# Performance work log

Hardware: AMD Instinct MI355X
Metric: run time of the kernel (lower is better)

## Reference

```python
import jax, jax.numpy as jnp
import numpy as np

# hyperparameters (from init_kwargs / repo defaults)
AMP_COEF = 1.0
ARG_COEF = 1.0
SSIM_COEF = 1.0
BETA = 1.0
STFT_COEF = 1e-4
EPS = 1e-8
STFT_F = 12
STFT_S = 4


def _gauss_kernel(size=11, sigma=1.5):
    x = jnp.arange(size, dtype=jnp.float32) - (size - 1) / 2.0
    g = jnp.exp(-0.5 * (x / sigma) ** 2)
    k = jnp.outer(g, g)
    return k / jnp.sum(k)


def _depthwise_filter(img, k):
    # img: [B,H,W,C]; 11x11 gaussian, VALID padding, depthwise (per-channel)
    c = img.shape[-1]
    kern = jnp.tile(k[:, :, None, None], (1, 1, 1, c))  # HWIO, I=1, O=C
    return jax.lax.conv_general_dilated(
        img, kern, (1, 1), 'VALID',
        dimension_numbers=('NHWC', 'HWIO', 'NHWC'),
        feature_group_count=c)


def ssim(x, y, max_val=1.0):
    # faithful to tf.image.ssim defaults: filter 11, sigma 1.5, k1=0.01, k2=0.03
    c1 = (0.01 * max_val) ** 2
    c2 = (0.03 * max_val) ** 2
    k = _gauss_kernel()
    mu_x = _depthwise_filter(x, k)
    mu_y = _depthwise_filter(y, k)
    var_x = _depthwise_filter(x * x, k) - mu_x * mu_x
    var_y = _depthwise_filter(y * y, k) - mu_y * mu_y
    cov = _depthwise_filter(x * y, k) - mu_x * mu_y
    lum = (2.0 * mu_x * mu_y + c1) / (mu_x * mu_x + mu_y * mu_y + c1)
    cs = (2.0 * cov + c2) / (var_x + var_y + c2)
    return jnp.mean(lum * cs, axis=(1, 2, 3))  # [B]


def stft(image, f=STFT_F, s=STFT_S):
    # image: [B,N,N,C] -> batched patchwise 2D FFT, cropped to [:f//2,:f//2]
    n = image.shape[1]
    p = (n - f) // s + 1          # num_conv per axis
    half = f // 2
    rows = (jnp.arange(p) * s)[:, None] + jnp.arange(f)   # [P, f]
    patches = image[:, rows]                              # [B,P,f,N,C]
    patches = patches[:, :, :, rows]                      # [B,P,f,P,f,C]
    patches = jnp.transpose(patches, (0, 1, 3, 2, 4, 5))  # [B,Pi,Pj,f,f,C]
    b, c = image.shape[0], image.shape[-1]
    patches = patches.reshape(b, p * p, f, f, c)          # k = i*P + j ordering
    fft = jnp.fft.fft2(patches.astype(jnp.complex64), axes=(2, 3))
    return fft[:, :, :half, :half, :]                     # [B,P*P,half,half,C]


def _freq_filter(f=STFT_F):
    lin = jnp.linspace(0.0, 1.0, f // 2)[:, None]
    return (lin * lin.T)[:, :, None]                      # [half,half,1]


def setup_inputs() -> dict:
    key = jax.random.key(0)
    k1, k2, k3, k4 = jax.random.split(key, 4)
    B, N, C, L = 32, 160, 3, 128
    return {
        'mean': jax.random.normal(k1, (B, L), dtype=jnp.float32),
        'logvar': jax.random.normal(k2, (B, L), dtype=jnp.float32),
        'x_in': jax.random.uniform(k3, (B, N, N, C), dtype=jnp.float32),
        'x_out': jax.random.uniform(k4, (B, N, N, C), dtype=jnp.float32),
    }


def reference(mean, logvar, x_in, x_out):
    # KLD per sample
    var = jnp.exp(logvar)
    kld = -0.5 * jnp.sum(1.0 + logvar - var - mean * mean, axis=1)  # [B]
    # SSIM recon term
    recons = SSIM_COEF * ssim(x_in, x_out, 1.0)                     # [B]
    # patchwise STFT amp/phase loss ('ours')
    stft_out = stft(x_out, STFT_F, STFT_S)
    stft_in = stft(x_in, STFT_F, STFT_S)
    ff = _freq_filter(STFT_F)                                       # [half,half,1]
    arg_diff = jnp.abs(jnp.angle(stft_out + EPS) - jnp.angle(stft_in + EPS))
    amp_diff = jnp.abs(jnp.abs(stft_out) - jnp.abs(stft_in))
    arg_loss = jnp.sum(arg_diff * ff, axis=(1, 2, 3, 4))            # [B]
    amp_loss = jnp.sum(amp_diff * ff, axis=(1, 2, 3, 4))            # [B]
    stft_loss = ARG_COEF * arg_loss + AMP_COEF * amp_loss
    loss = jnp.mean(BETA * kld + recons + STFT_COEF * stft_loss)
    return loss
```

## Files before the change

kernel.cpp:

```cpp
#include <hip/hip_runtime.h>
#include <hip/hip_fp16.h>
#include <math.h>

#define BATCH 32
#define NPIX 160
#define LDIM 128
#define OUT_SZ 150

#define THREADS 512
#define N_BLOCKS 1825
#define RD_OFF   2880
#define VPMU_OFF 2880
#define VPVV_OFF 4192
#define VPXY_OFF 5504
#define VROWSTR  164
#define SMEM_FLOATS 8960

__device__ constexpr float TWC[12] = { 1.f, 0.86602540f, 0.5f, 0.f, -0.5f, -0.86602540f,
                                      -1.f,-0.86602540f,-0.5f, 0.f,  0.5f,  0.86602540f};
__device__ constexpr float TWS[12] = { 0.f,-0.5f,-0.86602540f,-1.f,-0.86602540f,-0.5f,
                                       0.f, 0.5f, 0.86602540f, 1.f, 0.86602540f, 0.5f};

__device__ constexpr float GW[11] = {0.00102838f, 0.00759876f, 0.03600076f, 0.10936070f,
                                     0.21300554f, 0.26601172f, 0.21300554f, 0.10936070f,
                                     0.03600076f, 0.00759876f, 0.00102838f};

__device__ __forceinline__ float fast_atan2f(float y, float x) {
    float ax = fabsf(x), ay = fabsf(y);
    float mx = fmaxf(ax, ay), mn = fminf(ax, ay);
    float z = mn * __builtin_amdgcn_rcpf(mx);
    float z2 = z * z;
    float p = fmaf(z2, -0.01172120f, 0.05265332f);
    p = fmaf(z2, p, -0.11643287f);
    p = fmaf(z2, p, 0.19354346f);
    p = fmaf(z2, p, -0.33262347f);
    p = fmaf(z2, p, 0.99997726f);
    p = p * z;
    if (ay > ax) p = 1.57079632679489662f - p;
    if (x < 0.f) p = 3.14159265358979323f - p;
    return (y < 0.f) ? -p : p;
}

__device__ __forceinline__ __half2 h2swap(__half2 v) {
    unsigned u;
    __builtin_memcpy(&u, &v, 4);
    u = (u >> 16) | (u << 16);
    __half2 r;
    __builtin_memcpy(&r, &u, 4);
    return r;
}

__device__ __forceinline__ float4 extract_c(float4 f0, float4 f1, float4 f2, int c) {
    if (c == 0) return make_float4(f0.x, f0.w, f1.z, f2.y);
    if (c == 1) return make_float4(f0.y, f1.x, f1.w, f2.z);
    return make_float4(f0.z, f1.y, f2.x, f2.w);
}

__global__ __launch_bounds__(THREADS) void work_kernel(const float* __restrict__ xin,
                                                       const float* __restrict__ xout,
                                                       const float* __restrict__ mean,
                                                       const float* __restrict__ logvar,
                                                       float* __restrict__ out) {
    __shared__ __align__(16) float SMEM[SMEM_FLOATS];
    __shared__ float sm8[8];
    const int tid = threadIdx.x;
    const int gid = blockIdx.x;
    float acc = 0.f;

    if (gid == 1824) {
        float a = 0.f;
        for (int i = tid; i < BATCH * LDIM; i += THREADS) {
            float m = mean[i], lv = logvar[i];
            a += -0.5f * (1.f + lv - expf(lv) - m * m) * (1.f / 32.f);
        }
        #pragma unroll
        for (int o = 32; o > 0; o >>= 1) a += __shfl_down(a, o, 64);
        if ((tid & 63) == 0) sm8[tid >> 6] = a;
        __syncthreads();
        if (tid == 0) {
            float s = sm8[0];
            #pragma unroll
            for (int i = 1; i < 8; ++i) s += sm8[i];
            atomicAdd(out, s);
        }
        return;
    }

    int idx  = (gid & 7) * 228 + (gid >> 3);
    int b    = idx / 57;
    int rem  = idx % 57;
    int tile = (rem / 3);
    int c    = rem % 3;
    int r0 = tile * 8;
    __half2* HXY = (__half2*)SMEM;
    __half2* RD  = (__half2*)(SMEM + RD_OFF);
    const __half2 hz = __float2half2_rn(0.f);

    for (int t = tid; t < 720; t += THREADS) {
        int rr = t / 40;
        int cq = t % 40;
        int row = r0 + rr;
        float4 xa = make_float4(0.f, 0.f, 0.f, 0.f);
        float4 xb = make_float4(0.f, 0.f, 0.f, 0.f);
        if (row < NPIX) {
            size_t off = ((size_t)(b * 160 + row) * 160 + cq * 4) * 3;
            const float4* qa = (const float4*)(xin + off);
            const float4* qb = (const float4*)(xout + off);
            float4 a0 = qa[0], a1 = qa[1], a2 = qa[2];
            float4 b0 = qb[0], b1 = qb[1], b2 = qb[2];
            xa = extract_c(a0, a1, a2, c);
            xb = extract_c(b0, b1, b2, c);
        }
        __half2 h[4] __attribute__((aligned(16)));
        h[0] = __floats2half2_rn(xa.x, xb.x);
        h[1] = __floats2half2_rn(xa.y, xb.y);
        h[2] = __floats2half2_rn(xa.z, xb.z);
        h[3] = __floats2half2_rn(xa.w, xb.w);
        *(float4*)&HXY[rr * 160 + cq * 4] = *(float4*)h;
    }
    __syncthreads();

    for (int t = tid; t < 608; t += THREADS) {
        int pc = t % 38;
        int r  = t / 38;
        float4 raw[3];
        raw[0] = *(const float4*)&HXY[r * 160 + pc * 4];
        raw[1] = *(const float4*)&HXY[r * 160 + pc * 4 + 4];
        raw[2] = *(const float4*)&HXY[r * 160 + pc * 4 + 8];
        const __half2* x = (const __half2*)raw;
        __half2 ev[5], ov[5];
        #pragma unroll
        for (int j = 1; j <= 5; ++j) {
            ev[j-1] = __hadd2(x[j], x[12 - j]);
            ov[j-1] = __hsub2(x[j], x[12 - j]);
        }
        __half2* dst = &RD[(r * 38 + pc) * 10];
        #pragma unroll
        for (int vv = 0; vv < 5; ++vv) {
            const int v = vv + 1;
            __half2 re = (v & 1) ? __hsub2(x[0], x[6]) : __hadd2(x[0], x[6]);
            __half2 im = hz;
            #pragma unroll
            for (int j = 1; j <= 5; ++j) {
                const int kk = (v * j) % 12;
                re = __hfma2(ev[j-1], __float2half2_rn(TWC[kk]), re);
                im = __hfma2(ov[j-1], __float2half2_rn(TWS[kk]), im);
            }
            __half2 w2[2] __attribute__((aligned(8)));
            w2[0] = re;
            w2[1] = im;
            *(float2*)&dst[vv * 2] = *(float2*)w2;
        }
    }
    __syncthreads();

    if (tid < 380) {
        int pc = tid % 38;
        int vv = (tid / 38) % 5;
        int g  = tid / 190;
        __half2 FR[5], FI[5];
        #pragma unroll
        for (int uu = 0; uu < 5; ++uu) { FR[uu] = hz; FI[uu] = hz; }
        #pragma unroll
        for (int i = 0; i < 6; ++i) {
            int rlo = 4 * g + i, rhi = rlo + 6;
            __half2 lo[2] __attribute__((aligned(8)));
            __half2 hi[2] __attribute__((aligned(8)));
            *(float2*)lo = *(const float2*)&RD[(rlo * 38 + pc) * 10 + vv * 2];
            *(float2*)hi = *(const float2*)&RD[(rhi * 38 + pc) * 10 + vv * 2];
            __half2 spR = __hadd2(lo[0], hi[0]), smR = __hsub2(lo[0], hi[0]);
            __half2 spI = __hadd2(lo[1], hi[1]), smI = __hsub2(lo[1], hi[1]);
            #pragma unroll
            for (int uu = 0; uu < 5; ++uu) {
                const int u = uu + 1;
                const int kk = (u * i) % 12;
                __half2 sR = (u & 1) ? smR : spR;
                __half2 sI = (u & 1) ? smI : spI;
                FR[uu] = __hfma2(sR, __float2half2_rn(TWC[kk]),
                         __hfma2(sI, __float2half2_rn(-TWS[kk]), FR[uu]));
                FI[uu] = __hfma2(sI, __float2half2_rn(TWC[kk]),
                         __hfma2(sR, __float2half2_rn(TWS[kk]), FI[uu]));
            }
        }
        float sacc = 0.f;
        #pragma unroll
        for (int uu = 0; uu < 5; ++uu) {
            float2 fr = __half22float2(FR[uu]);
            float2 fi = __half22float2(FI[uu]);
            float aI = fast_atan2f(fi.x, fr.x + 1e-8f);
            float aO = fast_atan2f(fi.y, fr.y + 1e-8f);
            float mI = __builtin_amdgcn_sqrtf(fmaf(fr.x, fr.x, fi.x * fi.x));
            float mO = __builtin_amdgcn_sqrtf(fmaf(fr.y, fr.y, fi.y * fi.y));
            float ff = (float)((uu + 1) * (vv + 1)) * 0.04f;
            sacc += ff * (fabsf(aO - aI) + fabsf(mO - mI));
        }
        acc += sacc * (1e-4f / 32.f);
    }
    __syncthreads();

    for (int t = tid; t < 320; t += THREADS) {
        int orow = t / 40;
        int cbase = (t % 40) * 4;
        __half2 amu[4], avv[4], axy[4];
        #pragma unroll
        for (int o = 0; o < 4; ++o) { amu[o] = hz; avv[o] = hz; axy[o] = hz; }
        #pragma unroll
        for (int kk = 0; kk < 11; ++kk) {
            float4 raw = *(const float4*)&HXY[(orow + kk) * 160 + cbase];
            const __half2* h = (const __half2*)&raw;
            const __half2 w2 = __float2half2_rn(GW[kk]);
            #pragma unroll
            for (int o = 0; o < 4; ++o) {
                __half2 t2 = __hmul2(w2, h[o]);
                amu[o] = __hadd2(amu[o], t2);
                avv[o] = __hfma2(t2, h[o], avv[o]);
                axy[o] = __hfma2(t2, h2swap(h[o]), axy[o]);
            }
        }
        int base = orow * VROWSTR + cbase;
        *(float4*)&SMEM[VPMU_OFF + base] = *(float4*)amu;
        *(float4*)&SMEM[VPVV_OFF + base] = *(float4*)avv;
        *(float4*)&SMEM[VPXY_OFF + base] = make_float4(
            __low2float(axy[0]), __low2float(axy[1]),
            __low2float(axy[2]), __low2float(axy[3]));
    }
    __syncthreads();

    {
        float hacc = 0.f;
        for (int t = tid; t < 600; t += THREADS) {
            int orow = t / 75;
            int oc = (t % 75) * 2;
            int base = orow * VROWSTR + oc;
            __half2 m[12], s0 = hz, s1 = hz;
            #pragma unroll
            for (int q = 0; q < 6; ++q)
                *(float2*)&m[2 * q] = *(const float2*)&SMEM[VPMU_OFF + base + 2 * q];
            #pragma unroll
            for (int kk = 0; kk < 11; ++kk) {
                const __half2 w2 = __float2half2_rn(GW[kk]);
                s0 = __hfma2(w2, m[kk],     s0);
                s1 = __hfma2(w2, m[kk + 1], s1);
            }
            float2 mu0 = __half22float2(s0);
            float2 mu1 = __half22float2(s1);
            __half2 v0 = hz, v1 = hz;
            #pragma unroll
            for (int q = 0; q < 6; ++q)
                *(float2*)&m[2 * q] = *(const float2*)&SMEM[VPVV_OFF + base + 2 * q];
            #pragma unroll
            for (int kk = 0; kk < 11; ++kk) {
                const __half2 w2 = __float2half2_rn(GW[kk]);
                v0 = __hfma2(w2, m[kk],     v0);
                v1 = __hfma2(w2, m[kk + 1], v1);
            }
            float2 vv0 = __half22float2(v0);
            float2 vv1 = __half22float2(v1);
            float zs[12];
            #pragma unroll
            for (int q = 0; q < 6; ++q) {
                float2 y2 = *(const float2*)&SMEM[VPXY_OFF + base + 2 * q];
                zs[2 * q] = y2.x; zs[2 * q + 1] = y2.y;
            }
            float xy0 = 0.f, xy1 = 0.f;
            #pragma unroll
            for (int kk = 0; kk < 11; ++kk) {
                xy0 = fmaf(GW[kk], zs[kk],     xy0);
                xy1 = fmaf(GW[kk], zs[kk + 1], xy1);
            }
            if (r0 + orow < OUT_SZ) {
                const float c1 = 1e-4f, c2 = 9e-4f;
                #pragma unroll
                for (int o = 0; o < 2; ++o) {
                    float mx = o ? mu1.x : mu0.x, my = o ? mu1.y : mu0.y;
                    float ex = o ? vv1.x : vv0.x, ey = o ? vv1.y : vv0.y;
                    float cv = (o ? xy1 : xy0) - mx * my;
                    float vx = ex - mx * mx;
                    float vy = ey - my * my;
                    float lum = (2.f * mx * my + c1) *
                                __builtin_amdgcn_rcpf(fmaf(mx, mx, my * my) + c1);
                    float cs  = (2.f * cv + c2) *
                                __builtin_amdgcn_rcpf(vx + vy + c2);
                    hacc += lum * cs;
                }
            }
        }
        acc += hacc * (1.f / (32.f * 150.f * 150.f * 3.f));
    }

    #pragma unroll
    for (int o = 32; o > 0; o >>= 1) acc += __shfl_down(acc, o, 64);
    if ((tid & 63) == 0) sm8[tid >> 6] = acc;
    __syncthreads();
    if (tid == 0) {
        float s = sm8[0];
        #pragma unroll
        for (int i = 1; i < 8; ++i) s += sm8[i];
        atomicAdd(out, s);
    }
}

extern "C" void kernel_launch(void* const* d_in, const int* in_sizes, int n_in,
                              void* d_out, int out_size, void* d_ws, size_t ws_size,
                              hipStream_t stream) {
    const float* mean   = (const float*)d_in[0];
    const float* logvar = (const float*)d_in[1];
    const float* xin    = (const float*)d_in[2];
    const float* xout   = (const float*)d_in[3];
    float* out = (float*)d_out;

    hipMemsetAsync(out, 0, sizeof(float), stream);
    work_kernel<<<N_BLOCKS, THREADS, 0, stream>>>(xin, xout, mean, logvar, out);
}
```

Baseline: 105.2 us.

## Give each wavefront private shared-memory scratch and drop block-wide barriers between stages

After the block-wide load of the tile into shared memory, each wavefront now owns a fixed slice of patch columns and one SSIM output row. Each wavefront uses its own private shared-memory workspace, so the row-DFT, column-DFT, vertical and horizontal blur stages need only compiler memory fences instead of __syncthreads. The HXY row stride is padded to 164 to reduce bank conflicts. The phase difference is now taken from one atan2 of the conjugate product with wrap correction instead of two atan2 calls. This cuts barrier stalls and transcendental work, but the uneven per-wave work split (5 vs 4 columns) may leave some lanes idle, and relying on wave-synchronous execution without explicit wave barriers is a correctness risk.

```diff
diff --git a/kernel.cpp b/kernel.cpp
--- a/kernel.cpp
+++ b/kernel.cpp
@@ -9,12 +9,13 @@
 
 #define THREADS 512
 #define N_BLOCKS 1825
-#define RD_OFF   2880
-#define VPMU_OFF 2880
-#define VPVV_OFF 4192
-#define VPXY_OFF 5504
-#define VROWSTR  164
-#define SMEM_FLOATS 8960
+
+#define HXYSTR 164
+#define HXY_SZ (18 * HXYSTR)
+#define SMEM_FLOATS (HXY_SZ + 6 * 800 + 2 * 640)
+#define VP_MU 0
+#define VP_VV 160
+#define VP_XY 320
 
 __device__ constexpr float TWC[12] = { 1.f, 0.86602540f, 0.5f, 0.f, -0.5f, -0.86602540f,
                                       -1.f,-0.86602540f,-0.5f, 0.f,  0.5f,  0.86602540f};
@@ -89,11 +90,17 @@
     int idx  = (gid & 7) * 228 + (gid >> 3);
     int b    = idx / 57;
     int rem  = idx % 57;
-    int tile = (rem / 3);
+    int tile = rem / 3;
     int c    = rem % 3;
     int r0 = tile * 8;
+
     __half2* HXY = (__half2*)SMEM;
-    __half2* RD  = (__half2*)(SMEM + RD_OFF);
+    const int wid  = tid >> 6;
+    const int lane = tid & 63;
+    const int npcl = (wid < 6) ? 5 : 4;
+    const int pc0  = (wid < 6) ? wid * 5 : 30 + (wid - 6) * 4;
+    float*   WS  = SMEM + HXY_SZ + ((wid < 6) ? wid * 800 : 4800 + (wid - 6) * 640);
+    __half2* RDW = (__half2*)WS;
     const __half2 hz = __float2half2_rn(0.f);
 
     for (int t = tid; t < 720; t += THREADS) {
@@ -116,17 +123,19 @@
         h[1] = __floats2half2_rn(xa.y, xb.y);
         h[2] = __floats2half2_rn(xa.z, xb.z);
         h[3] = __floats2half2_rn(xa.w, xb.w);
-        *(float4*)&HXY[rr * 160 + cq * 4] = *(float4*)h;
+        *(float4*)&HXY[rr * HXYSTR + cq * 4] = *(float4*)h;
     }
     __syncthreads();
 
-    for (int t = tid; t < 608; t += THREADS) {
-        int pc = t % 38;
-        int r  = t / 38;
+    for (int t = lane; t < 16 * npcl; t += 64) {
+        int r, pcl;
+        if (npcl == 5) { r = t / 5;  pcl = t - r * 5; }
+        else           { r = t >> 2; pcl = t & 3; }
+        int pc = pc0 + pcl;
         float4 raw[3];
-        raw[0] = *(const float4*)&HXY[r * 160 + pc * 4];
-        raw[1] = *(const float4*)&HXY[r * 160 + pc * 4 + 4];
-        raw[2] = *(const float4*)&HXY[r * 160 + pc * 4 + 8];
+        raw[0] = *(const float4*)&HXY[r * HXYSTR + pc * 4];
+        raw[1] = *(const float4*)&HXY[r * HXYSTR + pc * 4 + 4];
+        raw[2] = *(const float4*)&HXY[r * HXYSTR + pc * 4 + 8];
         const __half2* x = (const __half2*)raw;
         __half2 ev[5], ov[5];
         #pragma unroll
@@ -134,7 +143,6 @@
             ev[j-1] = __hadd2(x[j], x[12 - j]);
             ov[j-1] = __hsub2(x[j], x[12 - j]);
         }
-        __half2* dst = &RD[(r * 38 + pc) * 10];
         #pragma unroll
         for (int vv = 0; vv < 5; ++vv) {
             const int v = vv + 1;
@@ -149,64 +157,75 @@
             __half2 w2[2] __attribute__((aligned(8)));
             w2[0] = re;
             w2[1] = im;
-            *(float2*)&dst[vv * 2] = *(float2*)w2;
-        }
-    }
-    __syncthreads();
-
-    if (tid < 380) {
-        int pc = tid % 38;
-        int vv = (tid / 38) % 5;
-        int g  = tid / 190;
-        __half2 FR[5], FI[5];
-        #pragma unroll
-        for (int uu = 0; uu < 5; ++uu) { FR[uu] = hz; FI[uu] = hz; }
-        #pragma unroll
-        for (int i = 0; i < 6; ++i) {
-            int rlo = 4 * g + i, rhi = rlo + 6;
-            __half2 lo[2] __attribute__((aligned(8)));
-            __half2 hi[2] __attribute__((aligned(8)));
-            *(float2*)lo = *(const float2*)&RD[(rlo * 38 + pc) * 10 + vv * 2];
-            *(float2*)hi = *(const float2*)&RD[(rhi * 38 + pc) * 10 + vv * 2];
-            __half2 spR = __hadd2(lo[0], hi[0]), smR = __hsub2(lo[0], hi[0]);
-            __half2 spI = __hadd2(lo[1], hi[1]), smI = __hsub2(lo[1], hi[1]);
+            *(float2*)&RDW[((r * 5 + vv) * npcl + pcl) * 2] = *(float2*)w2;
+        }
+    }
+    asm volatile("" ::: "memory");
+
+    {
+        int g = lane >> 5, j = lane & 31;
+        if (j < 5 * npcl) {
+            int vvq, pcl;
+            if (npcl == 5) { vvq = j / 5;  pcl = j - vvq * 5; }
+            else           { vvq = j >> 2; pcl = j & 3; }
+            __half2 FR[5], FI[5];
+            #pragma unroll
+            for (int uu = 0; uu < 5; ++uu) { FR[uu] = hz; FI[uu] = hz; }
+            #pragma unroll
+            for (int i = 0; i < 6; ++i) {
+                int rlo = 4 * g + i, rhi = rlo + 6;
+                __half2 lo[2] __attribute__((aligned(8)));
+                __half2 hi[2] __attribute__((aligned(8)));
+                *(float2*)lo = *(const float2*)&RDW[((rlo * 5 + vvq) * npcl + pcl) * 2];
+                *(float2*)hi = *(const float2*)&RDW[((rhi * 5 + vvq) * npcl + pcl) * 2];
+                __half2 spR = __hadd2(lo[0], hi[0]), smR = __hsub2(lo[0], hi[0]);
+                __half2 spI = __hadd2(lo[1], hi[1]), smI = __hsub2(lo[1], hi[1]);
+                #pragma unroll
+                for (int uu = 0; uu < 5; ++uu) {
+                    const int u = uu + 1;
+                    const int kk = (u * i) % 12;
+                    __half2 sR = (u & 1) ? smR : spR;
+                    __half2 sI = (u & 1) ? smI : spI;
+                    FR[uu] = __hfma2(sR, __float2half2_rn(TWC[kk]),
+                             __hfma2(sI, __float2half2_rn(-TWS[kk]), FR[uu]));
+                    FI[uu] = __hfma2(sI, __float2half2_rn(TWC[kk]),
+                             __hfma2(sR, __float2half2_rn(TWS[kk]), FI[uu]));
+                }
+            }
+            float sacc = 0.f;
             #pragma unroll
             for (int uu = 0; uu < 5; ++uu) {
-                const int u = uu + 1;
-                const int kk = (u * i) % 12;
-                __half2 sR = (u & 1) ? smR : spR;
-                __half2 sI = (u & 1) ? smI : spI;
-                FR[uu] = __hfma2(sR, __float2half2_rn(TWC[kk]),
-                         __hfma2(sI, __float2half2_rn(-TWS[kk]), FR[uu]));
-                FI[uu] = __hfma2(sI, __float2half2_rn(TWC[kk]),
-                         __hfma2(sR, __float2half2_rn(TWS[kk]), FI[uu]));
-            }
-        }
-        float sacc = 0.f;
-        #pragma unroll
-        for (int uu = 0; uu < 5; ++uu) {
-            float2 fr = __half22float2(FR[uu]);
-            float2 fi = __half22float2(FI[uu]);
-            float aI = fast_atan2f(fi.x, fr.x + 1e-8f);
-            float aO = fast_atan2f(fi.y, fr.y + 1e-8f);
-            float mI = __builtin_amdgcn_sqrtf(fmaf(fr.x, fr.x, fi.x * fi.x));
-            float mO = __builtin_amdgcn_sqrtf(fmaf(fr.y, fr.y, fi.y * fi.y));
-            float ff = (float)((uu + 1) * (vv + 1)) * 0.04f;
-            sacc += ff * (fabsf(aO - aI) + fabsf(mO - mI));
-        }
-        acc += sacc * (1e-4f / 32.f);
-    }
-    __syncthreads();
-
-    for (int t = tid; t < 320; t += THREADS) {
-        int orow = t / 40;
-        int cbase = (t % 40) * 4;
+                float2 fr = __half22float2(FR[uu]);
+                float2 fi = __half22float2(FI[uu]);
+                float rb = fr.x + 1e-8f, ib = fi.x;
+                float ra = fr.y + 1e-8f, ia = fi.y;
+                float re_p = fmaf(ra, rb, ia * ib);
+                float im_p = fmaf(ia, rb, -(ra * ib));
+                float w  = fast_atan2f(im_p, re_p);
+                float aw = fabsf(w);
+                float alt = 6.28318530717958648f - aw;
+                bool sa = (ia < 0.f), sb = (ib < 0.f);
+                float adiff = (sa == sb) ? aw
+                             : (((w >= 0.f) == !sa) ? aw : alt);
+                float mI = __builtin_amdgcn_sqrtf(fmaf(fr.x, fr.x, fi.x * fi.x));
+                float mO = __builtin_amdgcn_sqrtf(fmaf(fr.y, fr.y, fi.y * fi.y));
+                float ff = (float)((uu + 1) * (vvq + 1)) * 0.04f;
+                sacc += ff * (adiff + fabsf(mO - mI));
+            }
+            acc += sacc * (1e-4f / 32.f);
+        }
+    }
+    asm volatile("" ::: "memory");
+
+    if (lane < 40) {
+        const int orow = wid;
+        int cbase = lane * 4;
         __half2 amu[4], avv[4], axy[4];
         #pragma unroll
         for (int o = 0; o < 4; ++o) { amu[o] = hz; avv[o] = hz; axy[o] = hz; }
         #pragma unroll
         for (int kk = 0; kk < 11; ++kk) {
-            float4 raw = *(const float4*)&HXY[(orow + kk) * 160 + cbase];
+            float4 raw = *(const float4*)&HXY[(orow + kk) * HXYSTR + cbase];
             const __half2* h = (const __half2*)&raw;
             const __half2 w2 = __float2half2_rn(GW[kk]);
             #pragma unroll
@@ -217,25 +236,22 @@
                 axy[o] = __hfma2(t2, h2swap(h[o]), axy[o]);
             }
         }
-        int base = orow * VROWSTR + cbase;
-        *(float4*)&SMEM[VPMU_OFF + base] = *(float4*)amu;
-        *(float4*)&SMEM[VPVV_OFF + base] = *(float4*)avv;
-        *(float4*)&SMEM[VPXY_OFF + base] = make_float4(
+        *(float4*)&WS[VP_MU + cbase] = *(float4*)amu;
+        *(float4*)&WS[VP_VV + cbase] = *(float4*)avv;
+        *(float4*)&WS[VP_XY + cbase] = make_float4(
             __low2float(axy[0]), __low2float(axy[1]),
             __low2float(axy[2]), __low2float(axy[3]));
     }
-    __syncthreads();
-
-    {
+    asm volatile("" ::: "memory");
+
+    if (r0 + wid < OUT_SZ) {
         float hacc = 0.f;
-        for (int t = tid; t < 600; t += THREADS) {
-            int orow = t / 75;
-            int oc = (t % 75) * 2;
-            int base = orow * VROWSTR + oc;
+        for (int t = lane; t < 75; t += 64) {
+            int oc = t * 2;
             __half2 m[12], s0 = hz, s1 = hz;
             #pragma unroll
             for (int q = 0; q < 6; ++q)
-                *(float2*)&m[2 * q] = *(const float2*)&SMEM[VPMU_OFF + base + 2 * q];
+                *(float2*)&m[2 * q] = *(const float2*)&WS[VP_MU + oc + 2 * q];
             #pragma unroll
             for (int kk = 0; kk < 11; ++kk) {
                 const __half2 w2 = __float2half2_rn(GW[kk]);
@@ -247,7 +263,7 @@
             __half2 v0 = hz, v1 = hz;
             #pragma unroll
             for (int q = 0; q < 6; ++q)
-                *(float2*)&m[2 * q] = *(const float2*)&SMEM[VPVV_OFF + base + 2 * q];
+                *(float2*)&m[2 * q] = *(const float2*)&WS[VP_VV + oc + 2 * q];
             #pragma unroll
             for (int kk = 0; kk < 11; ++kk) {
                 const __half2 w2 = __float2half2_rn(GW[kk]);
@@ -259,7 +275,7 @@
             float zs[12];
             #pragma unroll
             for (int q = 0; q < 6; ++q) {
-                float2 y2 = *(const float2*)&SMEM[VPXY_OFF + base + 2 * q];
+                float2 y2 = *(const float2*)&WS[VP_XY + oc + 2 * q];
                 zs[2 * q] = y2.x; zs[2 * q + 1] = y2.y;
             }
             float xy0 = 0.f, xy1 = 0.f;
@@ -268,21 +284,19 @@
                 xy0 = fmaf(GW[kk], zs[kk],     xy0);
                 xy1 = fmaf(GW[kk], zs[kk + 1], xy1);
             }
-            if (r0 + orow < OUT_SZ) {
-                const float c1 = 1e-4f, c2 = 9e-4f;
-                #pragma unroll
-                for (int o = 0; o < 2; ++o) {
-                    float mx = o ? mu1.x : mu0.x, my = o ? mu1.y : mu0.y;
-                    float ex = o ? vv1.x : vv0.x, ey = o ? vv1.y : vv0.y;
-                    float cv = (o ? xy1 : xy0) - mx * my;
-                    float vx = ex - mx * mx;
-                    float vy = ey - my * my;
-                    float lum = (2.f * mx * my + c1) *
-                                __builtin_amdgcn_rcpf(fmaf(mx, mx, my * my) + c1);
-                    float cs  = (2.f * cv + c2) *
-                                __builtin_amdgcn_rcpf(vx + vy + c2);
-                    hacc += lum * cs;
-                }
+            const float c1 = 1e-4f, c2 = 9e-4f;
+            #pragma unroll
+            for (int o = 0; o < 2; ++o) {
+                float mx = o ? mu1.x : mu0.x, my = o ? mu1.y : mu0.y;
+                float ex = o ? vv1.x : vv0.x, ey = o ? vv1.y : vv0.y;
+                float cv = (o ? xy1 : xy0) - mx * my;
+                float vx = ex - mx * mx;
+                float vy = ey - my * my;
+                float lum = (2.f * mx * my + c1) *
+                            __builtin_amdgcn_rcpf(fmaf(mx, mx, my * my) + c1);
+                float cs  = (2.f * cv + c2) *
+                            __builtin_amdgcn_rcpf(vx + vy + c2);
+                hacc += lum * cs;
             }
         }
         acc += hacc * (1.f / (32.f * 150.f * 150.f * 3.f));
```

After: 106.2 us. About the same (+0.9%).

## Register-block SSIM separable passes over two rows and four columns per thread

Applied to the files above, without the earlier changes.

The vertical Gaussian pass now has each thread compute two adjacent output rows over two columns. It shares 12 loaded input rows between both instead of loading 11 rows per single output row. The horizontal pass gives each thread four consecutive outputs from 14 loaded values, cutting redundant LDS reads, and brings the work down to 304 tasks so it fits in one pass of the 512-thread block. The row stride of the intermediate buffers changes to 166 to alter bank mapping. The trade-off is more registers per thread and fewer active threads in the horizontal stage.

```diff
diff --git a/kernel.cpp b/kernel.cpp
--- a/kernel.cpp
+++ b/kernel.cpp
@@ -11,9 +11,9 @@
 #define N_BLOCKS 1825
 #define RD_OFF   2880
 #define VPMU_OFF 2880
-#define VPVV_OFF 4192
-#define VPXY_OFF 5504
-#define VROWSTR  164
+#define VPVV_OFF 4208
+#define VPXY_OFF 5536
+#define VROWSTR  166
 #define SMEM_FLOATS 8960
 
 __device__ constexpr float TWC[12] = { 1.f, 0.86602540f, 0.5f, 0.f, -0.5f, -0.86602540f,
@@ -89,7 +89,7 @@
     int idx  = (gid & 7) * 228 + (gid >> 3);
     int b    = idx / 57;
     int rem  = idx % 57;
-    int tile = (rem / 3);
+    int tile = rem / 3;
     int c    = rem % 3;
     int r0 = tile * 8;
     __half2* HXY = (__half2*)SMEM;
@@ -199,89 +199,117 @@
     __syncthreads();
 
     for (int t = tid; t < 320; t += THREADS) {
-        int orow = t / 40;
-        int cbase = (t % 40) * 4;
-        __half2 amu[4], avv[4], axy[4];
-        #pragma unroll
-        for (int o = 0; o < 4; ++o) { amu[o] = hz; avv[o] = hz; axy[o] = hz; }
-        #pragma unroll
-        for (int kk = 0; kk < 11; ++kk) {
-            float4 raw = *(const float4*)&HXY[(orow + kk) * 160 + cbase];
-            const __half2* h = (const __half2*)&raw;
-            const __half2 w2 = __float2half2_rn(GW[kk]);
-            #pragma unroll
-            for (int o = 0; o < 4; ++o) {
-                __half2 t2 = __hmul2(w2, h[o]);
-                amu[o] = __hadd2(amu[o], t2);
-                avv[o] = __hfma2(t2, h[o], avv[o]);
-                axy[o] = __hfma2(t2, h2swap(h[o]), axy[o]);
-            }
-        }
-        int base = orow * VROWSTR + cbase;
-        *(float4*)&SMEM[VPMU_OFF + base] = *(float4*)amu;
-        *(float4*)&SMEM[VPVV_OFF + base] = *(float4*)avv;
-        *(float4*)&SMEM[VPXY_OFF + base] = make_float4(
-            __low2float(axy[0]), __low2float(axy[1]),
-            __low2float(axy[2]), __low2float(axy[3]));
+        int op  = t / 80;
+        int cp  = t % 80;
+        int col = cp * 2;
+        __half2 amu[2][2], avv[2][2], axy[2][2];
+        #pragma unroll
+        for (int dr = 0; dr < 2; ++dr)
+            #pragma unroll
+            for (int o = 0; o < 2; ++o) { amu[dr][o] = hz; avv[dr][o] = hz; axy[dr][o] = hz; }
+        #pragma unroll
+        for (int kk = 0; kk < 12; ++kk) {
+            __half2 h2[2] __attribute__((aligned(8)));
+            *(float2*)h2 = *(const float2*)&HXY[(2 * op + kk) * 160 + col];
+            if (kk < 11) {
+                const __half2 w2 = __float2half2_rn(GW[kk]);
+                #pragma unroll
+                for (int o = 0; o < 2; ++o) {
+                    __half2 t2 = __hmul2(w2, h2[o]);
+                    amu[0][o] = __hadd2(amu[0][o], t2);
+                    avv[0][o] = __hfma2(t2, h2[o], avv[0][o]);
+                    axy[0][o] = __hfma2(t2, h2swap(h2[o]), axy[0][o]);
+                }
+            }
+            if (kk >= 1) {
+                const __half2 w2 = __float2half2_rn(GW[kk - 1]);
+                #pragma unroll
+                for (int o = 0; o < 2; ++o) {
+                    __half2 t2 = __hmul2(w2, h2[o]);
+                    amu[1][o] = __hadd2(amu[1][o], t2);
+                    avv[1][o] = __hfma2(t2, h2[o], avv[1][o]);
+                    axy[1][o] = __hfma2(t2, h2swap(h2[o]), axy[1][o]);
+                }
+            }
+        }
+        #pragma unroll
+        for (int dr = 0; dr < 2; ++dr) {
+            int base = (2 * op + dr) * VROWSTR + col;
+            __half2 pm[2] __attribute__((aligned(8)));
+            __half2 pv[2] __attribute__((aligned(8)));
+            pm[0] = amu[dr][0]; pm[1] = amu[dr][1];
+            pv[0] = avv[dr][0]; pv[1] = avv[dr][1];
+            *(float2*)&SMEM[VPMU_OFF + base] = *(float2*)pm;
+            *(float2*)&SMEM[VPVV_OFF + base] = *(float2*)pv;
+            *(float2*)&SMEM[VPXY_OFF + base] = make_float2(
+                __low2float(axy[dr][0]), __low2float(axy[dr][1]));
+        }
     }
     __syncthreads();
 
     {
         float hacc = 0.f;
-        for (int t = tid; t < 600; t += THREADS) {
-            int orow = t / 75;
-            int oc = (t % 75) * 2;
-            int base = orow * VROWSTR + oc;
-            __half2 m[12], s0 = hz, s1 = hz;
-            #pragma unroll
-            for (int q = 0; q < 6; ++q)
-                *(float2*)&m[2 * q] = *(const float2*)&SMEM[VPMU_OFF + base + 2 * q];
-            #pragma unroll
-            for (int kk = 0; kk < 11; ++kk) {
-                const __half2 w2 = __float2half2_rn(GW[kk]);
-                s0 = __hfma2(w2, m[kk],     s0);
-                s1 = __hfma2(w2, m[kk + 1], s1);
-            }
-            float2 mu0 = __half22float2(s0);
-            float2 mu1 = __half22float2(s1);
-            __half2 v0 = hz, v1 = hz;
-            #pragma unroll
-            for (int q = 0; q < 6; ++q)
-                *(float2*)&m[2 * q] = *(const float2*)&SMEM[VPVV_OFF + base + 2 * q];
-            #pragma unroll
-            for (int kk = 0; kk < 11; ++kk) {
-                const __half2 w2 = __float2half2_rn(GW[kk]);
-                v0 = __hfma2(w2, m[kk],     v0);
-                v1 = __hfma2(w2, m[kk + 1], v1);
-            }
-            float2 vv0 = __half22float2(v0);
-            float2 vv1 = __half22float2(v1);
-            float zs[12];
-            #pragma unroll
-            for (int q = 0; q < 6; ++q) {
-                float2 y2 = *(const float2*)&SMEM[VPXY_OFF + base + 2 * q];
-                zs[2 * q] = y2.x; zs[2 * q + 1] = y2.y;
-            }
-            float xy0 = 0.f, xy1 = 0.f;
-            #pragma unroll
-            for (int kk = 0; kk < 11; ++kk) {
-                xy0 = fmaf(GW[kk], zs[kk],     xy0);
-                xy1 = fmaf(GW[kk], zs[kk + 1], xy1);
+        for (int t = tid; t < 304; t += THREADS) {
+            int orow = t & 7;
+            int wgrp = t >> 3;
+            int w0 = wgrp * 4;
+            int rbase = orow * VROWSTR + w0;
+            __half2 mv[14];
+            #pragma unroll
+            for (int q = 0; q < 7; ++q)
+                *(float2*)&mv[2 * q] = *(const float2*)&SMEM[VPMU_OFF + rbase + 2 * q];
+            __half2 ms[4];
+            #pragma unroll
+            for (int k = 0; k < 4; ++k) {
+                __half2 s = hz;
+                #pragma unroll
+                for (int j = 0; j < 11; ++j)
+                    s = __hfma2(__float2half2_rn(GW[j]), mv[k + j], s);
+                ms[k] = s;
+            }
+            #pragma unroll
+            for (int q = 0; q < 7; ++q)
+                *(float2*)&mv[2 * q] = *(const float2*)&SMEM[VPVV_OFF + rbase + 2 * q];
+            __half2 vs[4];
+            #pragma unroll
+            for (int k = 0; k < 4; ++k) {
+                __half2 s = hz;
+                #pragma unroll
+                for (int j = 0; j < 11; ++j)
+                    s = __hfma2(__float2half2_rn(GW[j]), mv[k + j], s);
+                vs[k] = s;
+            }
+            float xv[14];
+            #pragma unroll
+            for (int q = 0; q < 7; ++q) {
+                float2 y2 = *(const float2*)&SMEM[VPXY_OFF + rbase + 2 * q];
+                xv[2 * q] = y2.x; xv[2 * q + 1] = y2.y;
+            }
+            float xs[4];
+            #pragma unroll
+            for (int k = 0; k < 4; ++k) {
+                float s = 0.f;
+                #pragma unroll
+                for (int j = 0; j < 11; ++j)
+                    s = fmaf(GW[j], xv[k + j], s);
+                xs[k] = s;
             }
             if (r0 + orow < OUT_SZ) {
                 const float c1 = 1e-4f, c2 = 9e-4f;
                 #pragma unroll
-                for (int o = 0; o < 2; ++o) {
-                    float mx = o ? mu1.x : mu0.x, my = o ? mu1.y : mu0.y;
-                    float ex = o ? vv1.x : vv0.x, ey = o ? vv1.y : vv0.y;
-                    float cv = (o ? xy1 : xy0) - mx * my;
-                    float vx = ex - mx * mx;
-                    float vy = ey - my * my;
-                    float lum = (2.f * mx * my + c1) *
-                                __builtin_amdgcn_rcpf(fmaf(mx, mx, my * my) + c1);
-                    float cs  = (2.f * cv + c2) *
-                                __builtin_amdgcn_rcpf(vx + vy + c2);
-                    hacc += lum * cs;
+                for (int k = 0; k < 4; ++k) {
+                    if (w0 + k < OUT_SZ) {
+                        float2 mu = __half22float2(ms[k]);
+                        float2 v2 = __half22float2(vs[k]);
+                        float cv = xs[k] - mu.x * mu.y;
+                        float vx = v2.x - mu.x * mu.x;
+                        float vy = v2.y - mu.y * mu.y;
+                        float lum = (2.f * mu.x * mu.y + c1) *
+                                    __builtin_amdgcn_rcpf(fmaf(mu.x, mu.x, mu.y * mu.y) + c1);
+                        float cs  = (2.f * cv + c2) *
+                                    __builtin_amdgcn_rcpf(vx + vy + c2);
+                        hacc += lum * cs;
+                    }
                 }
             }
         }
```

New measurement: 105.1 us. About the same (-0.1%).
